# Performance work log

Measured on AMD Instinct MI355X. Metric: run time of the kernel, lower is better.

The kernel has to match this reference:

```python
import jax, jax.numpy as jnp
import numpy as np

N_NODES = 100000
N_EDGES = 3200000


def _cheb_norm(edge_index, edge_weight, num_nodes):
    # PyG ChebConv.__norm__ with normalization='sym', lambda_max=2.0:
    # L_hat = 2/lambda_max * (I - D^-1/2 A D^-1/2) - I = -D^-1/2 A D^-1/2
    # (the +1 diagonal from get_laplacian and the -1 self-loops cancel),
    # so only the off-diagonal terms -d_i^-1/2 w_ij d_j^-1/2 remain.
    src, dst = edge_index[0], edge_index[1]
    deg = jax.ops.segment_sum(edge_weight, src, num_segments=num_nodes)
    safe = jnp.where(deg > 0, deg, 1.0)
    dis = jnp.where(deg > 0, jax.lax.rsqrt(safe), 0.0)  # deg_inv_sqrt, inf -> 0
    return -dis[src] * edge_weight * dis[dst]


def _cheb_conv(x, src, dst, norm, W, b, num_nodes):
    # W: [K, C_in, C_out]. Chebyshev recurrence Tx_k = 2 L_hat Tx_{k-1} - Tx_{k-2}.
    def prop(h):  # (L_hat h)[dst] += norm_e * h[src]
        return jax.ops.segment_sum(norm[:, None] * h[src], dst, num_segments=num_nodes)

    K = W.shape[0]
    out = x @ W[0]
    if K > 1:
        tx1 = prop(x)
        out = out + tx1 @ W[1]
        if K > 2:
            def step(carry, Wk):
                tx_m2, tx_m1, acc = carry
                tx = 2.0 * prop(tx_m1) - tx_m2
                return (tx_m1, tx, acc + tx @ Wk), None
            (_, _, out), _ = jax.lax.scan(step, (x, tx1, out), W[2:])
    if b is not None:
        out = out + b
    return out


def setup_inputs() -> dict:
    key = jax.random.key(0)
    ks = jax.random.split(key, 12)
    x = jax.random.normal(ks[0], (N_NODES, 2), dtype=jnp.float32)
    edge_index = jax.random.randint(ks[1], (2, N_EDGES), 0, N_NODES, dtype=jnp.int64)
    edge_weight = jax.random.uniform(ks[2], (N_EDGES,), dtype=jnp.float32)
    s = 0.1  # keep activations in a sane range (glorot-ish scale)
    W1 = jax.random.normal(ks[3], (39, 2, 14), dtype=jnp.float32) * s
    b1 = jax.random.normal(ks[4], (14,), dtype=jnp.float32) * s
    W2 = jax.random.normal(ks[5], (43, 14, 20), dtype=jnp.float32) * s
    b2 = jax.random.normal(ks[6], (20,), dtype=jnp.float32) * s
    W3 = jax.random.normal(ks[7], (45, 20, 27), dtype=jnp.float32) * s
    b3 = jax.random.normal(ks[8], (27,), dtype=jnp.float32) * s
    W4 = jax.random.normal(ks[9], (1, 27, 1), dtype=jnp.float32) * s  # K=1, no bias
    return {"x": x, "edge_index": edge_index, "edge_weight": edge_weight,
            "W1": W1, "b1": b1, "W2": W2, "b2": b2, "W3": W3, "b3": b3, "W4": W4}


def reference(x, edge_index, edge_weight, W1, b1, W2, b2, W3, b3, W4):
    src, dst = edge_index[0], edge_index[1]
    norm = _cheb_norm(edge_index, edge_weight, N_NODES)
    h = jax.nn.silu(_cheb_conv(x, src, dst, norm, W1, b1, N_NODES))
    h = jax.nn.silu(_cheb_conv(h, src, dst, norm, W2, b2, N_NODES))
    h = jax.nn.silu(_cheb_conv(h, src, dst, norm, W3, b3, N_NODES))
    h = _cheb_conv(h, src, dst, norm, W4, None, N_NODES)
    return jax.nn.sigmoid(h)
```

## Files before the change

### kernel.cpp

```cpp
#include <hip/hip_runtime.h>
#include <math.h>

#define N_NODES 100000
#define N_EDGES 3200000
#define BS 256
#define CAP_SHIFT 7
#define CAP (1 << CAP_SHIFT)


__global__ void scan_partial_kernel(const int* __restrict__ cnt, int* __restrict__ bsums) {
    __shared__ int lds[256];
    int tid = threadIdx.x;
    int base = blockIdx.x * 1024 + tid * 4;
    int s = 0;
#pragma unroll
    for (int i = 0; i < 4; ++i) s += (base + i < N_NODES) ? cnt[base + i] : 0;
    lds[tid] = s;
    __syncthreads();
    for (int off = 128; off > 0; off >>= 1) {
        if (tid < off) lds[tid] += lds[tid + off];
        __syncthreads();
    }
    if (tid == 0) bsums[blockIdx.x] = lds[0];
}

__global__ void scan_bsums_kernel(int* __restrict__ bsums, int nb, int* __restrict__ total_out) {
    if (threadIdx.x == 0 && blockIdx.x == 0) {
        int acc = 0;
        for (int b = 0; b < nb; ++b) {
            int v = bsums[b];
            bsums[b] = acc;
            acc += v;
        }
        *total_out = acc;
    }
}

__global__ void scan_final_kernel(const int* __restrict__ cnt, const int* __restrict__ bsums,
                                  int* __restrict__ rp) {
    __shared__ int lds[256];
    int tid = threadIdx.x;
    int base = blockIdx.x * 1024 + tid * 4;
    int v[4];
    int ts = 0;
#pragma unroll
    for (int i = 0; i < 4; ++i) {
        v[i] = (base + i < N_NODES) ? cnt[base + i] : 0;
        ts += v[i];
    }
    lds[tid] = ts;
    __syncthreads();
    for (int off = 1; off < 256; off <<= 1) {
        int t = (tid >= off) ? lds[tid - off] : 0;
        __syncthreads();
        lds[tid] += t;
        __syncthreads();
    }
    int run = lds[tid] - ts + bsums[blockIdx.x];
#pragma unroll
    for (int i = 0; i < 4; ++i) {
        if (base + i < N_NODES) rp[base + i] = run;
        run += v[i];
    }
}

__global__ void fill_direct_kernel(const int* __restrict__ src, const int* __restrict__ dst,
                                   int* __restrict__ cnt_s, int* __restrict__ cnt_d,
                                   int* __restrict__ bkt_s, int* __restrict__ bkt_d) {
    int e = blockIdx.x * blockDim.x + threadIdx.x;
    if (e >= N_EDGES) return;
    int s = src[e];
    int d = dst[e];
    int slot_s = atomicAdd(&cnt_s[s], 1);
    bkt_s[((size_t)s << CAP_SHIFT) + slot_s] = e;
    int slot_d = atomicAdd(&cnt_d[d], 1);
    bkt_d[((size_t)d << CAP_SHIFT) + slot_d] = e;
}

__global__ __launch_bounds__(64) void sort_deg_dis_kernel(
    const int* __restrict__ cnt, const int* __restrict__ bkt,
    const float* __restrict__ w, float* __restrict__ dis) {
#pragma clang fp contract(off)
    {
        __shared__ int lr[64][65];
        __shared__ int ls[64][65];
        int n = blockIdx.x * 64 + threadIdx.x;
        if (n >= N_NODES) return;
        int c = cnt[n];
        const int* row = bkt + ((size_t)n << CAP_SHIFT);
        float d = 0.f;
        if (c <= 64) {
            int* a = lr[threadIdx.x];
            int* b = ls[threadIdx.x];
            for (int i = 0; i < c; ++i) a[i] = row[i];
            for (int i = 0; i < c; ++i) {
                int v = a[i];
                int rk = 0;
                for (int j = 0; j < c; ++j) rk += (a[j] < v);
                b[rk] = v;
            }
            for (int r = 0; r < c; ++r) d = d + w[b[r]];
        } else {
            for (int r = 0; r < c; ++r) {
                for (int i = 0; i < c; ++i) {
                    int v = row[i];
                    int rk = 0;
                    for (int j = 0; j < c; ++j) rk += (row[j] < v);
                    if (rk == r) { d = d + w[v]; break; }
                }
            }
        }
        dis[n] = (d > 0.f) ? (1.0f / sqrtf(d)) : 0.f;
    }
}

__global__ __launch_bounds__(64) void sort_pack_kernel(
    const int* __restrict__ cnt, const int* __restrict__ rp,
    const int* __restrict__ bkt, const int* __restrict__ src,
    const float* __restrict__ w, const float* __restrict__ dis,
    int2* __restrict__ packed) {
#pragma clang fp contract(off)
    {
        __shared__ int lr[64][65];
        __shared__ int ls[64][65];
        int n = blockIdx.x * 64 + threadIdx.x;
        if (n >= N_NODES) return;
        int c = cnt[n];
        const int* row = bkt + ((size_t)n << CAP_SHIFT);
        int beg = rp[n];
        float din = dis[n];
        if (c <= 64) {
            int* a = lr[threadIdx.x];
            int* b = ls[threadIdx.x];
            for (int i = 0; i < c; ++i) a[i] = row[i];
            for (int i = 0; i < c; ++i) {
                int v = a[i];
                int rk = 0;
                for (int j = 0; j < c; ++j) rk += (a[j] < v);
                b[rk] = v;
            }
            for (int r = 0; r < c; ++r) {
                int e = b[r];
                int s = src[e];
                float cw = ((-dis[s]) * w[e]) * din;
                packed[beg + r] = make_int2(s, __float_as_int(cw));
            }
        } else {
            for (int r = 0; r < c; ++r) {
                for (int i = 0; i < c; ++i) {
                    int v = row[i];
                    int rk = 0;
                    for (int j = 0; j < c; ++j) rk += (row[j] < v);
                    if (rk == r) {
                        int s = src[v];
                        float cw = ((-dis[s]) * w[v]) * din;
                        packed[beg + r] = make_int2(s, __float_as_int(cw));
                        break;
                    }
                }
            }
        }
    }
}


template <int CIN, int COUT, int SIN, int SACC>
__global__ void layer_init_kernel(const float* __restrict__ hin, const float* __restrict__ W0,
                                  float* __restrict__ acc) {
    int t = blockIdx.x * blockDim.x + threadIdx.x;
    if (t >= N_NODES * COUT) return;
    int n = t / COUT, co = t - n * COUT;
    const float* hr = hin + (size_t)n * SIN;
    float m = 0.f;
#pragma unroll
    for (int ci = 0; ci < CIN; ++ci) m = fmaf(hr[ci], W0[ci * COUT + co], m);
    acc[(size_t)n * SACC + co] = m;
}

template <int CIN, int COUT, int SIN, int SACC, int GS, int LANES, int R>
__global__ __launch_bounds__(LANES* R) void prop_mm_kernel(
    const int* __restrict__ rp, const int2* __restrict__ pk, const float* __restrict__ hin,
    const float* __restrict__ prev, const float* __restrict__ Wk, int rec,
    float* __restrict__ tx_out, float* __restrict__ acc) {
#pragma clang fp contract(off)
    {
        __shared__ float tls[R][LANES * GS];
        int r = threadIdx.x / LANES;
        int lane = threadIdx.x - r * LANES;
        int n = blockIdx.x * R + r;
        bool vn = (n < N_NODES);
        if (vn) {
            int c0 = lane * GS;
            float s[GS];
#pragma unroll
            for (int g = 0; g < GS; ++g) s[g] = 0.f;
            int beg = rp[n], end = rp[n + 1];
            int j = beg;
            if constexpr (GS == 4) {
                for (; j + 7 < end; j += 8) {
                    int2 p0 = pk[j];
                    int2 p1 = pk[j + 1];
                    int2 p2 = pk[j + 2];
                    int2 p3 = pk[j + 3];
                    int2 p4 = pk[j + 4];
                    int2 p5 = pk[j + 5];
                    int2 p6 = pk[j + 6];
                    int2 p7 = pk[j + 7];
                    const float4 q0 = *reinterpret_cast<const float4*>(hin + (size_t)p0.x * SIN + c0);
                    const float4 q1 = *reinterpret_cast<const float4*>(hin + (size_t)p1.x * SIN + c0);
                    const float4 q2 = *reinterpret_cast<const float4*>(hin + (size_t)p2.x * SIN + c0);
                    const float4 q3 = *reinterpret_cast<const float4*>(hin + (size_t)p3.x * SIN + c0);
                    const float4 q4 = *reinterpret_cast<const float4*>(hin + (size_t)p4.x * SIN + c0);
                    const float4 q5 = *reinterpret_cast<const float4*>(hin + (size_t)p5.x * SIN + c0);
                    const float4 q6 = *reinterpret_cast<const float4*>(hin + (size_t)p6.x * SIN + c0);
                    const float4 q7 = *reinterpret_cast<const float4*>(hin + (size_t)p7.x * SIN + c0);
                    float w0 = __int_as_float(p0.y), w1 = __int_as_float(p1.y);
                    float w2 = __int_as_float(p2.y), w3 = __int_as_float(p3.y);
                    float w4 = __int_as_float(p4.y), w5 = __int_as_float(p5.y);
                    float w6 = __int_as_float(p6.y), w7 = __int_as_float(p7.y);
                    s[0] = s[0] + (w0 * q0.x); s[1] = s[1] + (w0 * q0.y);
                    s[2] = s[2] + (w0 * q0.z); s[3] = s[3] + (w0 * q0.w);
                    s[0] = s[0] + (w1 * q1.x); s[1] = s[1] + (w1 * q1.y);
                    s[2] = s[2] + (w1 * q1.z); s[3] = s[3] + (w1 * q1.w);
                    s[0] = s[0] + (w2 * q2.x); s[1] = s[1] + (w2 * q2.y);
                    s[2] = s[2] + (w2 * q2.z); s[3] = s[3] + (w2 * q2.w);
                    s[0] = s[0] + (w3 * q3.x); s[1] = s[1] + (w3 * q3.y);
                    s[2] = s[2] + (w3 * q3.z); s[3] = s[3] + (w3 * q3.w);
                    s[0] = s[0] + (w4 * q4.x); s[1] = s[1] + (w4 * q4.y);
                    s[2] = s[2] + (w4 * q4.z); s[3] = s[3] + (w4 * q4.w);
                    s[0] = s[0] + (w5 * q5.x); s[1] = s[1] + (w5 * q5.y);
                    s[2] = s[2] + (w5 * q5.z); s[3] = s[3] + (w5 * q5.w);
                    s[0] = s[0] + (w6 * q6.x); s[1] = s[1] + (w6 * q6.y);
                    s[2] = s[2] + (w6 * q6.z); s[3] = s[3] + (w6 * q6.w);
                    s[0] = s[0] + (w7 * q7.x); s[1] = s[1] + (w7 * q7.y);
                    s[2] = s[2] + (w7 * q7.z); s[3] = s[3] + (w7 * q7.w);
                }
                for (; j + 3 < end; j += 4) {
                    int2 p0 = pk[j];
                    int2 p1 = pk[j + 1];
                    int2 p2 = pk[j + 2];
                    int2 p3 = pk[j + 3];
                    const float4 q0 = *reinterpret_cast<const float4*>(hin + (size_t)p0.x * SIN + c0);
                    const float4 q1 = *reinterpret_cast<const float4*>(hin + (size_t)p1.x * SIN + c0);
                    const float4 q2 = *reinterpret_cast<const float4*>(hin + (size_t)p2.x * SIN + c0);
                    const float4 q3 = *reinterpret_cast<const float4*>(hin + (size_t)p3.x * SIN + c0);
                    float w0 = __int_as_float(p0.y), w1 = __int_as_float(p1.y);
                    float w2 = __int_as_float(p2.y), w3 = __int_as_float(p3.y);
                    s[0] = s[0] + (w0 * q0.x); s[1] = s[1] + (w0 * q0.y);
                    s[2] = s[2] + (w0 * q0.z); s[3] = s[3] + (w0 * q0.w);
                    s[0] = s[0] + (w1 * q1.x); s[1] = s[1] + (w1 * q1.y);
                    s[2] = s[2] + (w1 * q1.z); s[3] = s[3] + (w1 * q1.w);
                    s[0] = s[0] + (w2 * q2.x); s[1] = s[1] + (w2 * q2.y);
                    s[2] = s[2] + (w2 * q2.z); s[3] = s[3] + (w2 * q2.w);
                    s[0] = s[0] + (w3 * q3.x); s[1] = s[1] + (w3 * q3.y);
                    s[2] = s[2] + (w3 * q3.z); s[3] = s[3] + (w3 * q3.w);
                }
                for (; j < end; ++j) {
                    int2 p = pk[j];
                    float w = __int_as_float(p.y);
                    const float4 q = *reinterpret_cast<const float4*>(hin + (size_t)p.x * SIN + c0);
                    s[0] = s[0] + (w * q.x); s[1] = s[1] + (w * q.y);
                    s[2] = s[2] + (w * q.z); s[3] = s[3] + (w * q.w);
                }
            } else {
                for (; j + 7 < end; j += 8) {
                    int2 p0 = pk[j];
                    int2 p1 = pk[j + 1];
                    int2 p2 = pk[j + 2];
                    int2 p3 = pk[j + 3];
                    int2 p4 = pk[j + 4];
                    int2 p5 = pk[j + 5];
                    int2 p6 = pk[j + 6];
                    int2 p7 = pk[j + 7];
                    const float2 q0 = *reinterpret_cast<const float2*>(hin + (size_t)p0.x * SIN + c0);
                    const float2 q1 = *reinterpret_cast<const float2*>(hin + (size_t)p1.x * SIN + c0);
                    const float2 q2 = *reinterpret_cast<const float2*>(hin + (size_t)p2.x * SIN + c0);
                    const float2 q3 = *reinterpret_cast<const float2*>(hin + (size_t)p3.x * SIN + c0);
                    const float2 q4 = *reinterpret_cast<const float2*>(hin + (size_t)p4.x * SIN + c0);
                    const float2 q5 = *reinterpret_cast<const float2*>(hin + (size_t)p5.x * SIN + c0);
                    const float2 q6 = *reinterpret_cast<const float2*>(hin + (size_t)p6.x * SIN + c0);
                    const float2 q7 = *reinterpret_cast<const float2*>(hin + (size_t)p7.x * SIN + c0);
                    float w0 = __int_as_float(p0.y), w1 = __int_as_float(p1.y);
                    float w2 = __int_as_float(p2.y), w3 = __int_as_float(p3.y);
                    float w4 = __int_as_float(p4.y), w5 = __int_as_float(p5.y);
                    float w6 = __int_as_float(p6.y), w7 = __int_as_float(p7.y);
                    s[0] = s[0] + (w0 * q0.x); s[1] = s[1] + (w0 * q0.y);
                    s[0] = s[0] + (w1 * q1.x); s[1] = s[1] + (w1 * q1.y);
                    s[0] = s[0] + (w2 * q2.x); s[1] = s[1] + (w2 * q2.y);
                    s[0] = s[0] + (w3 * q3.x); s[1] = s[1] + (w3 * q3.y);
                    s[0] = s[0] + (w4 * q4.x); s[1] = s[1] + (w4 * q4.y);
                    s[0] = s[0] + (w5 * q5.x); s[1] = s[1] + (w5 * q5.y);
                    s[0] = s[0] + (w6 * q6.x); s[1] = s[1] + (w6 * q6.y);
                    s[0] = s[0] + (w7 * q7.x); s[1] = s[1] + (w7 * q7.y);
                }
                for (; j + 3 < end; j += 4) {
                    int2 p0 = pk[j];
                    int2 p1 = pk[j + 1];
                    int2 p2 = pk[j + 2];
                    int2 p3 = pk[j + 3];
                    const float2 q0 = *reinterpret_cast<const float2*>(hin + (size_t)p0.x * SIN + c0);
                    const float2 q1 = *reinterpret_cast<const float2*>(hin + (size_t)p1.x * SIN + c0);
                    const float2 q2 = *reinterpret_cast<const float2*>(hin + (size_t)p2.x * SIN + c0);
                    const float2 q3 = *reinterpret_cast<const float2*>(hin + (size_t)p3.x * SIN + c0);
                    float w0 = __int_as_float(p0.y), w1 = __int_as_float(p1.y);
                    float w2 = __int_as_float(p2.y), w3 = __int_as_float(p3.y);
                    s[0] = s[0] + (w0 * q0.x); s[1] = s[1] + (w0 * q0.y);
                    s[0] = s[0] + (w1 * q1.x); s[1] = s[1] + (w1 * q1.y);
                    s[0] = s[0] + (w2 * q2.x); s[1] = s[1] + (w2 * q2.y);
                    s[0] = s[0] + (w3 * q3.x); s[1] = s[1] + (w3 * q3.y);
                }
                for (; j < end; ++j) {
                    int2 p = pk[j];
                    float w = __int_as_float(p.y);
                    const float2 q = *reinterpret_cast<const float2*>(hin + (size_t)p.x * SIN + c0);
                    s[0] = s[0] + (w * q.x); s[1] = s[1] + (w * q.y);
                }
            }
            float t[GS];
            if (rec) {
#pragma unroll
                for (int g = 0; g < GS; ++g) t[g] = 2.f * s[g] - prev[(size_t)n * SIN + c0 + g];
            } else {
#pragma unroll
                for (int g = 0; g < GS; ++g) t[g] = s[g];
            }
#pragma unroll
            for (int g = 0; g < GS; ++g) tls[r][c0 + g] = t[g];
            if constexpr (GS == 4) {
                *reinterpret_cast<float4*>(tx_out + (size_t)n * SIN + c0) =
                    make_float4(t[0], t[1], t[2], t[3]);
            } else {
                *reinterpret_cast<float2*>(tx_out + (size_t)n * SIN + c0) =
                    make_float2(t[0], t[1]);
            }
        }
        __syncthreads();
        if (vn) {
            for (int co = lane; co < COUT; co += LANES) {
                float m = 0.f;
#pragma unroll
                for (int ci = 0; ci < CIN; ++ci) m = fmaf(tls[r][ci], Wk[ci * COUT + co], m);
                acc[(size_t)n * SACC + co] = acc[(size_t)n * SACC + co] + m;
            }
        }
    }
}

template <int C, int S>
__global__ void silu_bias_kernel(float* __restrict__ a, const float* __restrict__ b) {
#pragma clang fp contract(off)
    {
        int t = blockIdx.x * blockDim.x + threadIdx.x;
        if (t >= N_NODES * C) return;
        int n = t / C, c = t - n * C;
        float x = a[(size_t)n * S + c] + b[c];
        float sig = 1.f / (1.f + expf(-x));
        a[(size_t)n * S + c] = x * sig;
    }
}

__global__ void final_kernel(const float* __restrict__ acc, const float* __restrict__ b3,
                             const float* __restrict__ W4, float* __restrict__ out) {
#pragma clang fp contract(off)
    {
        int n = blockIdx.x * blockDim.x + threadIdx.x;
        if (n >= N_NODES) return;
        float m = 0.f;
#pragma unroll
        for (int ci = 0; ci < 27; ++ci) {
            float xv = acc[(size_t)n * 28 + ci] + b3[ci];
            float sig = 1.f / (1.f + expf(-xv));
            float hv = xv * sig;
            m = fmaf(hv, W4[ci], m);
        }
        out[n] = 1.f / (1.f + expf(-m));
    }
}

__global__ void signal_kernel(float* __restrict__ out, float val) {
    int n = blockIdx.x * blockDim.x + threadIdx.x;
    if (n < N_NODES) out[n] = val;
}


static void run_scan(const int* cnt, int* bsums, int* rp, hipStream_t stream) {
    const int nb = (N_NODES + 1023) / 1024;
    scan_partial_kernel<<<nb, 256, 0, stream>>>(cnt, bsums);
    scan_bsums_kernel<<<1, 64, 0, stream>>>(bsums, nb, rp + N_NODES);
    scan_final_kernel<<<nb, 256, 0, stream>>>(cnt, bsums, rp);
}

template <int CIN, int COUT, int SIN, int SACC, int GS, int LANES, int R>
static void run_layer(int K, const float* hin, const float* W, float* acc, float* b0, float* b1,
                      float* b2, const int* rp, const int2* pk, hipStream_t stream) {
    const int gInit = (N_NODES * COUT + BS - 1) / BS;
    const int gProp = (N_NODES + R - 1) / R;
    layer_init_kernel<CIN, COUT, SIN, SACC><<<gInit, BS, 0, stream>>>(hin, W, acc);
    if (K > 1) {
        float* bufs[3] = {b0, b1, b2};
        prop_mm_kernel<CIN, COUT, SIN, SACC, GS, LANES, R><<<gProp, LANES * R, 0, stream>>>(
            rp, pk, hin, nullptr, W + 1 * CIN * COUT, 0, bufs[0], acc);
        const float* pm2 = hin;
        const float* pm1 = bufs[0];
        for (int k = 2; k < K; ++k) {
            float* outb = bufs[(k - 1) % 3];
            prop_mm_kernel<CIN, COUT, SIN, SACC, GS, LANES, R><<<gProp, LANES * R, 0, stream>>>(
                rp, pk, pm1, pm2, W + k * CIN * COUT, 1, outb, acc);
            pm2 = pm1;
            pm1 = outb;
        }
    }
}

extern "C" void kernel_launch(void* const* d_in, const int* in_sizes, int n_in, void* d_out,
                              int out_size, void* d_ws, size_t ws_size, hipStream_t stream) {
    const float* x  = (const float*)d_in[0];
    const int* idx  = (const int*)d_in[1];
    const float* ew = (const float*)d_in[2];
    const float* W1 = (const float*)d_in[3];
    const float* b1 = (const float*)d_in[4];
    const float* W2 = (const float*)d_in[5];
    const float* b2 = (const float*)d_in[6];
    const float* W3 = (const float*)d_in[7];
    const float* b3 = (const float*)d_in[8];
    const float* W4 = (const float*)d_in[9];
    float* out = (float*)d_out;
    (void)in_sizes; (void)n_in; (void)out_size;

    const int* src = idx;
    const int* dst = idx + N_EDGES;

    size_t off = 0;
    auto alloc = [&](size_t bytes) {
        size_t o = off;
        off = (off + bytes + 255) & ~(size_t)255;
        return o;
    };
    char* ws = (char*)d_ws;
    int*   cnt_s   = (int*)(ws + alloc(N_NODES * 4));
    int*   cnt_d   = (int*)(ws + alloc(N_NODES * 4));
    int*   rp_src  = (int*)(ws + alloc((N_NODES + 1) * 4));
    int*   rp_dst  = (int*)(ws + alloc((N_NODES + 1) * 4));
    float* dis     = (float*)(ws + alloc(N_NODES * 4));
    int*   bsums   = (int*)(ws + alloc(512));
    int2*  packed  = (int2*)(ws + alloc((size_t)N_EDGES * 8));
    float* t0      = (float*)(ws + alloc((size_t)N_NODES * 20 * 4));
    float* t1      = (float*)(ws + alloc((size_t)N_NODES * 20 * 4));
    float* t2      = (float*)(ws + alloc((size_t)N_NODES * 20 * 4));
    float* accA    = (float*)(ws + alloc((size_t)N_NODES * 16 * 4));
    float* accB    = (float*)(ws + alloc((size_t)N_NODES * 20 * 4));
    float* accC    = (float*)(ws + alloc((size_t)N_NODES * 28 * 4));
    int*   bkt_s   = (int*)(ws + alloc((size_t)N_NODES * CAP * 4));
    int*   bkt_d   = (int*)(ws + alloc((size_t)N_NODES * CAP * 4));
    const size_t NEED = off;

    int gE = (N_EDGES + BS - 1) / BS;
    int gN = (N_NODES + BS - 1) / BS;
    const int gSort = (N_NODES + 63) / 64;

    if (ws_size < NEED) {
        signal_kernel<<<gN, BS, 0, stream>>>(
            out, 6000.0f + (float)(ws_size / (1024.0 * 1024.0)));
        return;
    }

    (void)hipMemsetAsync(cnt_s, 0, N_NODES * 4, stream);
    (void)hipMemsetAsync(cnt_d, 0, N_NODES * 4, stream);
    fill_direct_kernel<<<gE, BS, 0, stream>>>(src, dst, cnt_s, cnt_d, bkt_s, bkt_d);
    run_scan(cnt_s, bsums, rp_src, stream);
    run_scan(cnt_d, bsums, rp_dst, stream);
    sort_deg_dis_kernel<<<gSort, 64, 0, stream>>>(cnt_s, bkt_s, ew, dis);
    sort_pack_kernel<<<gSort, 64, 0, stream>>>(cnt_d, rp_dst, bkt_d, src, ew, dis, packed);

    run_layer<2, 14, 2, 16, 2, 1, 256>(39, x, W1, accA, t0, t1, t2, rp_dst, packed, stream);
    silu_bias_kernel<14, 16><<<(N_NODES * 14 + BS - 1) / BS, BS, 0, stream>>>(accA, b1);
    run_layer<14, 20, 16, 20, 4, 4, 64>(43, accA, W2, accB, t0, t1, t2, rp_dst, packed, stream);
    silu_bias_kernel<20, 20><<<(N_NODES * 20 + BS - 1) / BS, BS, 0, stream>>>(accB, b2);
    run_layer<20, 27, 20, 28, 4, 5, 51>(45, accB, W3, accC, t0, t1, t2, rp_dst, packed, stream);
    final_kernel<<<gN, BS, 0, stream>>>(accC, b3, W4, out);
}
```

Baseline: 7.692 ms.

## Split 20-channel layer-3 features into 16+4 planar layout for aligned float4 gathers

After: 8.111 ms. 5.4% more time.

```diff
diff --git a/kernel.cpp b/kernel.cpp
--- a/kernel.cpp
+++ b/kernel.cpp
@@ -6,6 +6,7 @@
 #define BS 256
 #define CAP_SHIFT 7
 #define CAP (1 << CAP_SHIFT)
+#define OFF2 1600000
 
 
 __global__ void scan_partial_kernel(const int* __restrict__ cnt, int* __restrict__ bsums) {
@@ -163,21 +164,47 @@
     }
 }
 
-
-template <int CIN, int COUT, int SIN, int SACC>
-__global__ void layer_init_kernel(const float* __restrict__ hin, const float* __restrict__ W0,
-                                  float* __restrict__ acc) {
+__device__ __forceinline__ size_t addrS(int n, int c) {
+    return (c < 16) ? ((size_t)n * 16 + c) : (OFF2 + (size_t)n * 4 + (c - 16));
+}
+
+
+__global__ void init1_kernel(const float* __restrict__ hin, const float* __restrict__ W0,
+                             float* __restrict__ acc) {
     int t = blockIdx.x * blockDim.x + threadIdx.x;
-    if (t >= N_NODES * COUT) return;
-    int n = t / COUT, co = t - n * COUT;
-    const float* hr = hin + (size_t)n * SIN;
+    if (t >= N_NODES * 14) return;
+    int n = t / 14, co = t - n * 14;
+    const float* hr = hin + (size_t)n * 2;
     float m = 0.f;
-#pragma unroll
-    for (int ci = 0; ci < CIN; ++ci) m = fmaf(hr[ci], W0[ci * COUT + co], m);
-    acc[(size_t)n * SACC + co] = m;
-}
-
-template <int CIN, int COUT, int SIN, int SACC, int GS, int LANES, int R>
+    m = fmaf(hr[0], W0[co], m);
+    m = fmaf(hr[1], W0[14 + co], m);
+    acc[(size_t)n * 16 + co] = m;
+}
+
+__global__ void init2_kernel(const float* __restrict__ hin, const float* __restrict__ W0,
+                             float* __restrict__ acc) {
+    int t = blockIdx.x * blockDim.x + threadIdx.x;
+    if (t >= N_NODES * 20) return;
+    int n = t / 20, co = t - n * 20;
+    const float* hr = hin + (size_t)n * 16;
+    float m = 0.f;
+#pragma unroll
+    for (int ci = 0; ci < 14; ++ci) m = fmaf(hr[ci], W0[ci * 20 + co], m);
+    acc[addrS(n, co)] = m;
+}
+
+__global__ void init3_kernel(const float* __restrict__ hin, const float* __restrict__ W0,
+                             float* __restrict__ acc) {
+    int t = blockIdx.x * blockDim.x + threadIdx.x;
+    if (t >= N_NODES * 27) return;
+    int n = t / 27, co = t - n * 27;
+    float m = 0.f;
+#pragma unroll
+    for (int ci = 0; ci < 20; ++ci) m = fmaf(hin[addrS(n, ci)], W0[ci * 27 + co], m);
+    acc[(size_t)n * 28 + co] = m;
+}
+
+template <int CIN, int COUT, int SIN, int SACC, int GS, int LANES, int R, int ACCSPLIT>
 __global__ __launch_bounds__(LANES* R) void prop_mm_kernel(
     const int* __restrict__ rp, const int2* __restrict__ pk, const float* __restrict__ hin,
     const float* __restrict__ prev, const float* __restrict__ Wk, int rec,
@@ -340,22 +367,186 @@
                 float m = 0.f;
 #pragma unroll
                 for (int ci = 0; ci < CIN; ++ci) m = fmaf(tls[r][ci], Wk[ci * COUT + co], m);
-                acc[(size_t)n * SACC + co] = acc[(size_t)n * SACC + co] + m;
-            }
-        }
-    }
-}
-
-template <int C, int S>
-__global__ void silu_bias_kernel(float* __restrict__ a, const float* __restrict__ b) {
+                size_t a;
+                if constexpr (ACCSPLIT) a = addrS(n, co);
+                else a = (size_t)n * SACC + co;
+                acc[a] = acc[a] + m;
+            }
+        }
+    }
+}
+
+__global__ __launch_bounds__(255) void prop_l3_kernel(
+    const int* __restrict__ rp, const int2* __restrict__ pk, const float* __restrict__ hin,
+    const float* __restrict__ prev, const float* __restrict__ Wk, int rec,
+    float* __restrict__ tx_out, float* __restrict__ acc) {
 #pragma clang fp contract(off)
     {
+        __shared__ float tls[51][20];
+        int r = threadIdx.x / 5;
+        int lane = threadIdx.x - r * 5;
+        int n = blockIdx.x * 51 + r;
+        bool vn = (n < N_NODES) && (r < 51);
+        if (vn) {
+            int beg = rp[n], end = rp[n + 1];
+            float s[4] = {0.f, 0.f, 0.f, 0.f};
+            float t[4];
+            if (lane < 4) {
+                int c0 = lane * 4;
+                int j = beg;
+                for (; j + 7 < end; j += 8) {
+                    int2 p0 = pk[j];
+                    int2 p1 = pk[j + 1];
+                    int2 p2 = pk[j + 2];
+                    int2 p3 = pk[j + 3];
+                    int2 p4 = pk[j + 4];
+                    int2 p5 = pk[j + 5];
+                    int2 p6 = pk[j + 6];
+                    int2 p7 = pk[j + 7];
+                    const float4 q0 = *reinterpret_cast<const float4*>(hin + (size_t)p0.x * 16 + c0);
+                    const float4 q1 = *reinterpret_cast<const float4*>(hin + (size_t)p1.x * 16 + c0);
+                    const float4 q2 = *reinterpret_cast<const float4*>(hin + (size_t)p2.x * 16 + c0);
+                    const float4 q3 = *reinterpret_cast<const float4*>(hin + (size_t)p3.x * 16 + c0);
+                    const float4 q4 = *reinterpret_cast<const float4*>(hin + (size_t)p4.x * 16 + c0);
+                    const float4 q5 = *reinterpret_cast<const float4*>(hin + (size_t)p5.x * 16 + c0);
+                    const float4 q6 = *reinterpret_cast<const float4*>(hin + (size_t)p6.x * 16 + c0);
+                    const float4 q7 = *reinterpret_cast<const float4*>(hin + (size_t)p7.x * 16 + c0);
+                    float w0 = __int_as_float(p0.y), w1 = __int_as_float(p1.y);
+                    float w2 = __int_as_float(p2.y), w3 = __int_as_float(p3.y);
+                    float w4 = __int_as_float(p4.y), w5 = __int_as_float(p5.y);
+                    float w6 = __int_as_float(p6.y), w7 = __int_as_float(p7.y);
+                    s[0] = s[0] + (w0 * q0.x); s[1] = s[1] + (w0 * q0.y);
+                    s[2] = s[2] + (w0 * q0.z); s[3] = s[3] + (w0 * q0.w);
+                    s[0] = s[0] + (w1 * q1.x); s[1] = s[1] + (w1 * q1.y);
+                    s[2] = s[2] + (w1 * q1.z); s[3] = s[3] + (w1 * q1.w);
+                    s[0] = s[0] + (w2 * q2.x); s[1] = s[1] + (w2 * q2.y);
+                    s[2] = s[2] + (w2 * q2.z); s[3] = s[3] + (w2 * q2.w);
+                    s[0] = s[0] + (w3 * q3.x); s[1] = s[1] + (w3 * q3.y);
+                    s[2] = s[2] + (w3 * q3.z); s[3] = s[3] + (w3 * q3.w);
+                    s[0] = s[0] + (w4 * q4.x); s[1] = s[1] + (w4 * q4.y);
+                    s[2] = s[2] + (w4 * q4.z); s[3] = s[3] + (w4 * q4.w);
+                    s[0] = s[0] + (w5 * q5.x); s[1] = s[1] + (w5 * q5.y);
+                    s[2] = s[2] + (w5 * q5.z); s[3] = s[3] + (w5 * q5.w);
+                    s[0] = s[0] + (w6 * q6.x); s[1] = s[1] + (w6 * q6.y);
+                    s[2] = s[2] + (w6 * q6.z); s[3] = s[3] + (w6 * q6.w);
+                    s[0] = s[0] + (w7 * q7.x); s[1] = s[1] + (w7 * q7.y);
+                    s[2] = s[2] + (w7 * q7.z); s[3] = s[3] + (w7 * q7.w);
+                }
+                for (; j < end; ++j) {
+                    int2 p = pk[j];
+                    float w = __int_as_float(p.y);
+                    const float4 q = *reinterpret_cast<const float4*>(hin + (size_t)p.x * 16 + c0);
+                    s[0] = s[0] + (w * q.x); s[1] = s[1] + (w * q.y);
+                    s[2] = s[2] + (w * q.z); s[3] = s[3] + (w * q.w);
+                }
+                size_t base = (size_t)n * 16 + c0;
+                if (rec) {
+                    const float4 pv = *reinterpret_cast<const float4*>(prev + base);
+                    t[0] = 2.f * s[0] - pv.x; t[1] = 2.f * s[1] - pv.y;
+                    t[2] = 2.f * s[2] - pv.z; t[3] = 2.f * s[3] - pv.w;
+                } else {
+                    t[0] = s[0]; t[1] = s[1]; t[2] = s[2]; t[3] = s[3];
+                }
+#pragma unroll
+                for (int g = 0; g < 4; ++g) tls[r][c0 + g] = t[g];
+                *reinterpret_cast<float4*>(tx_out + base) = make_float4(t[0], t[1], t[2], t[3]);
+            } else {
+                const float* hb = hin + OFF2;
+                int j = beg;
+                for (; j + 7 < end; j += 8) {
+                    int2 p0 = pk[j];
+                    int2 p1 = pk[j + 1];
+                    int2 p2 = pk[j + 2];
+                    int2 p3 = pk[j + 3];
+                    int2 p4 = pk[j + 4];
+                    int2 p5 = pk[j + 5];
+                    int2 p6 = pk[j + 6];
+                    int2 p7 = pk[j + 7];
+                    const float4 q0 = *reinterpret_cast<const float4*>(hb + (size_t)p0.x * 4);
+                    const float4 q1 = *reinterpret_cast<const float4*>(hb + (size_t)p1.x * 4);
+                    const float4 q2 = *reinterpret_cast<const float4*>(hb + (size_t)p2.x * 4);
+                    const float4 q3 = *reinterpret_cast<const float4*>(hb + (size_t)p3.x * 4);
+                    const float4 q4 = *reinterpret_cast<const float4*>(hb + (size_t)p4.x * 4);
+                    const float4 q5 = *reinterpret_cast<const float4*>(hb + (size_t)p5.x * 4);
+                    const float4 q6 = *reinterpret_cast<const float4*>(hb + (size_t)p6.x * 4);
+                    const float4 q7 = *reinterpret_cast<const float4*>(hb + (size_t)p7.x * 4);
+                    float w0 = __int_as_float(p0.y), w1 = __int_as_float(p1.y);
+                    float w2 = __int_as_float(p2.y), w3 = __int_as_float(p3.y);
+                    float w4 = __int_as_float(p4.y), w5 = __int_as_float(p5.y);
+                    float w6 = __int_as_float(p6.y), w7 = __int_as_float(p7.y);
+                    s[0] = s[0] + (w0 * q0.x); s[1] = s[1] + (w0 * q0.y);
+                    s[2] = s[2] + (w0 * q0.z); s[3] = s[3] + (w0 * q0.w);
+                    s[0] = s[0] + (w1 * q1.x); s[1] = s[1] + (w1 * q1.y);
+                    s[2] = s[2] + (w1 * q1.z); s[3] = s[3] + (w1 * q1.w);
+                    s[0] = s[0] + (w2 * q2.x); s[1] = s[1] + (w2 * q2.y);
+                    s[2] = s[2] + (w2 * q2.z); s[3] = s[3] + (w2 * q2.w);
+                    s[0] = s[0] + (w3 * q3.x); s[1] = s[1] + (w3 * q3.y);
+                    s[2] = s[2] + (w3 * q3.z); s[3] = s[3] + (w3 * q3.w);
+                    s[0] = s[0] + (w4 * q4.x); s[1] = s[1] + (w4 * q4.y);
+                    s[2] = s[2] + (w4 * q4.z); s[3] = s[3] + (w4 * q4.w);
+                    s[0] = s[0] + (w5 * q5.x); s[1] = s[1] + (w5 * q5.y);
+                    s[2] = s[2] + (w5 * q5.z); s[3] = s[3] + (w5 * q5.w);
+                    s[0] = s[0] + (w6 * q6.x); s[1] = s[1] + (w6 * q6.y);
+                    s[2] = s[2] + (w6 * q6.z); s[3] = s[3] + (w6 * q6.w);
+                    s[0] = s[0] + (w7 * q7.x); s[1] = s[1] + (w7 * q7.y);
+                    s[2] = s[2] + (w7 * q7.z); s[3] = s[3] + (w7 * q7.w);
+                }
+                for (; j < end; ++j) {
+                    int2 p = pk[j];
+                    float w = __int_as_float(p.y);
+                    const float4 q = *reinterpret_cast<const float4*>(hb + (size_t)p.x * 4);
+                    s[0] = s[0] + (w * q.x); s[1] = s[1] + (w * q.y);
+                    s[2] = s[2] + (w * q.z); s[3] = s[3] + (w * q.w);
+                }
+                size_t base = OFF2 + (size_t)n * 4;
+                if (rec) {
+                    const float4 pv = *reinterpret_cast<const float4*>(prev + base);
+                    t[0] = 2.f * s[0] - pv.x; t[1] = 2.f * s[1] - pv.y;
+                    t[2] = 2.f * s[2] - pv.z; t[3] = 2.f * s[3] - pv.w;
+                } else {
+                    t[0] = s[0]; t[1] = s[1]; t[2] = s[2]; t[3] = s[3];
+                }
+#pragma unroll
+                for (int g = 0; g < 4; ++g) tls[r][16 + g] = t[g];
+                *reinterpret_cast<float4*>(tx_out + base) = make_float4(t[0], t[1], t[2], t[3]);
+            }
+        }
+        __syncthreads();
+        if (vn) {
+            for (int co = lane; co < 27; co += 5) {
+                float m = 0.f;
+#pragma unroll
+                for (int ci = 0; ci < 20; ++ci) m = fmaf(tls[r][ci], Wk[ci * 27 + co], m);
+                size_t a = (size_t)n * 28 + co;
+                acc[a] = acc[a] + m;
+            }
+        }
+    }
+}
+
+__global__ void silu1_kernel(float* __restrict__ a, const float* __restrict__ b) {
+#pragma clang fp contract(off)
+    {
         int t = blockIdx.x * blockDim.x + threadIdx.x;
-        if (t >= N_NODES * C) return;
-        int n = t / C, c = t - n * C;
-        float x = a[(size_t)n * S + c] + b[c];
+        if (t >= N_NODES * 14) return;
+        int n = t / 14, c = t - n * 14;
+        size_t ad = (size_t)n * 16 + c;
+        float x = a[ad] + b[c];
         float sig = 1.f / (1.f + expf(-x));
-        a[(size_t)n * S + c] = x * sig;
+        a[ad] = x * sig;
+    }
+}
+
+__global__ void silu2_kernel(float* __restrict__ a, const float* __restrict__ b) {
+#pragma clang fp contract(off)
+    {
+        int t = blockIdx.x * blockDim.x + threadIdx.x;
+        if (t >= N_NODES * 20) return;
+        int n = t / 20, c = t - n * 20;
+        size_t ad = addrS(n, c);
+        float x = a[ad] + b[c];
+        float sig = 1.f / (1.f + expf(-x));
+        a[ad] = x * sig;
     }
 }
 
@@ -388,28 +579,6 @@
     scan_partial_kernel<<<nb, 256, 0, stream>>>(cnt, bsums);
     scan_bsums_kernel<<<1, 64, 0, stream>>>(bsums, nb, rp + N_NODES);
     scan_final_kernel<<<nb, 256, 0, stream>>>(cnt, bsums, rp);
-}
-
-template <int CIN, int COUT, int SIN, int SACC, int GS, int LANES, int R>
-static void run_layer(int K, const float* hin, const float* W, float* acc, float* b0, float* b1,
-                      float* b2, const int* rp, const int2* pk, hipStream_t stream) {
-    const int gInit = (N_NODES * COUT + BS - 1) / BS;
-    const int gProp = (N_NODES + R - 1) / R;
-    layer_init_kernel<CIN, COUT, SIN, SACC><<<gInit, BS, 0, stream>>>(hin, W, acc);
-    if (K > 1) {
-        float* bufs[3] = {b0, b1, b2};
-        prop_mm_kernel<CIN, COUT, SIN, SACC, GS, LANES, R><<<gProp, LANES * R, 0, stream>>>(
-            rp, pk, hin, nullptr, W + 1 * CIN * COUT, 0, bufs[0], acc);
-        const float* pm2 = hin;
-        const float* pm1 = bufs[0];
-        for (int k = 2; k < K; ++k) {
-            float* outb = bufs[(k - 1) % 3];
-            prop_mm_kernel<CIN, COUT, SIN, SACC, GS, LANES, R><<<gProp, LANES * R, 0, stream>>>(
-                rp, pk, pm1, pm2, W + k * CIN * COUT, 1, outb, acc);
-            pm2 = pm1;
-            pm1 = outb;
-        }
-    }
 }
 
 extern "C" void kernel_launch(void* const* d_in, const int* in_sizes, int n_in, void* d_out,
@@ -472,10 +641,51 @@
     sort_deg_dis_kernel<<<gSort, 64, 0, stream>>>(cnt_s, bkt_s, ew, dis);
     sort_pack_kernel<<<gSort, 64, 0, stream>>>(cnt_d, rp_dst, bkt_d, src, ew, dis, packed);
 
-    run_layer<2, 14, 2, 16, 2, 1, 256>(39, x, W1, accA, t0, t1, t2, rp_dst, packed, stream);
-    silu_bias_kernel<14, 16><<<(N_NODES * 14 + BS - 1) / BS, BS, 0, stream>>>(accA, b1);
-    run_layer<14, 20, 16, 20, 4, 4, 64>(43, accA, W2, accB, t0, t1, t2, rp_dst, packed, stream);
-    silu_bias_kernel<20, 20><<<(N_NODES * 20 + BS - 1) / BS, BS, 0, stream>>>(accB, b2);
-    run_layer<20, 27, 20, 28, 4, 5, 51>(45, accB, W3, accC, t0, t1, t2, rp_dst, packed, stream);
+    init1_kernel<<<(N_NODES * 14 + BS - 1) / BS, BS, 0, stream>>>(x, W1, accA);
+    {
+        float* bufs[3] = {t0, t1, t2};
+        const float* pm1 = x;
+        const float* pm2 = nullptr;
+        const int gProp = (N_NODES + 255) / 256;
+        for (int k = 1; k < 39; ++k) {
+            float* outb = bufs[(k - 1) % 3];
+            prop_mm_kernel<2, 14, 2, 16, 2, 1, 256, 0><<<gProp, 256, 0, stream>>>(
+                rp_dst, packed, pm1, pm2, W1 + (size_t)k * 2 * 14, (k >= 2) ? 1 : 0, outb, accA);
+            pm2 = pm1;
+            pm1 = outb;
+        }
+    }
+    silu1_kernel<<<(N_NODES * 14 + BS - 1) / BS, BS, 0, stream>>>(accA, b1);
+
+    init2_kernel<<<(N_NODES * 20 + BS - 1) / BS, BS, 0, stream>>>(accA, W2, accB);
+    {
+        float* bufs[3] = {t0, t1, t2};
+        const float* pm1 = accA;
+        const float* pm2 = nullptr;
+        const int gProp = (N_NODES + 63) / 64;
+        for (int k = 1; k < 43; ++k) {
+            float* outb = bufs[(k - 1) % 3];
+            prop_mm_kernel<14, 20, 16, 20, 4, 4, 64, 1><<<gProp, 256, 0, stream>>>(
+                rp_dst, packed, pm1, pm2, W2 + (size_t)k * 14 * 20, (k >= 2) ? 1 : 0, outb, accB);
+            pm2 = pm1;
+            pm1 = outb;
+        }
+    }
+    silu2_kernel<<<(N_NODES * 20 + BS - 1) / BS, BS, 0, stream>>>(accB, b2);
+
+    init3_kernel<<<(N_NODES * 27 + BS - 1) / BS, BS, 0, stream>>>(accB, W3, accC);
+    {
+        float* bufs[3] = {t0, t1, t2};
+        const float* pm1 = accB;
+        const float* pm2 = nullptr;
+        const int gProp = (N_NODES + 50) / 51;
+        for (int k = 1; k < 45; ++k) {
+            float* outb = bufs[(k - 1) % 3];
+            prop_l3_kernel<<<gProp, 255, 0, stream>>>(
+                rp_dst, packed, pm1, pm2, W3 + (size_t)k * 20 * 27, (k >= 2) ? 1 : 0, outb, accC);
+            pm2 = pm1;
+            pm1 = outb;
+        }
+    }
     final_kernel<<<gN, BS, 0, stream>>>(accC, b3, W4, out);
 }
```
